# Optimization experiments

Hardware: AMD Instinct MI355X
Metric: run time of the kernel (lower is better)

The kernel has to match this reference:

```python
import jax, jax.numpy as jnp
import numpy as np
from jax import lax

B, H, W = 2, 240, 1216
ITER, NUM = 3, 9
CH = ITER * NUM  # 27


def setup_inputs() -> dict:
    key = jax.random.key(0)
    ks = jax.random.split(key, 6)
    inp = jax.random.normal(ks[0], (B, 1, H, W), dtype=jnp.float32)
    guide = jax.random.normal(ks[1], (B, CH, H, W), dtype=jnp.float32)
    sp_dep = jax.random.uniform(ks[2], (B, 1, H, W), dtype=jnp.float32)
    confidence = jax.random.normal(ks[3], (B, 1, H, W), dtype=jnp.float32)
    conv_w = jax.random.normal(ks[4], (3 * CH, CH, 3, 3), dtype=jnp.float32) * 0.05
    conv_b = jax.random.normal(ks[5], (3 * CH,), dtype=jnp.float32) * 0.05
    # fixed 3x3 tap offsets, rows are (dx, dy) -- matches mode='xy'
    tap = jnp.array([[-1, -1], [0, -1], [1, -1], [-1, 0], [0, 0], [1, 0], [-1, 1], [0, 1], [1, 1]], dtype=jnp.float32)
    return {"input": inp, "guide": guide, "sp_dep": sp_dep, "confidence": confidence,
            "conv_w": conv_w, "conv_b": conv_b, "tap": tap}


def _bilinear_zeros(img, px, py):
    """img: [B,H,W]; px,py: [B,N,H,W] pixel coords. Matches F.grid_sample
    (bilinear, padding_mode='zeros', align_corners=False): the normalized grid
    built in get_refgrid maps exactly to pixel coord = x + tap + offset."""
    Hh, Ww = img.shape[-2], img.shape[-1]
    x0f = jnp.floor(px)
    y0f = jnp.floor(py)
    wx1 = px - x0f
    wy1 = py - y0f
    x0 = x0f.astype(jnp.int32)
    y0 = y0f.astype(jnp.int32)
    flat = img.reshape(img.shape[0], Hh * Ww)

    def gather(xi, yi):
        valid = (xi >= 0) & (xi < Ww) & (yi >= 0) & (yi < Hh)
        idx = jnp.clip(yi, 0, Hh - 1) * Ww + jnp.clip(xi, 0, Ww - 1)
        v = jax.vmap(lambda f, i: f[i])(flat, idx)  # [B,N,H,W]
        return jnp.where(valid, v, jnp.zeros((), img.dtype))

    v00 = gather(x0, y0)
    v01 = gather(x0 + 1, y0)
    v10 = gather(x0, y0 + 1)
    v11 = gather(x0 + 1, y0 + 1)
    return ((1 - wy1) * ((1 - wx1) * v00 + wx1 * v01)
            + wy1 * ((1 - wx1) * v10 + wx1 * v11))


def reference(input, guide, sp_dep, confidence, conv_w, conv_b, tap):
    Bb, _, Hh, Ww = input.shape
    out = lax.conv_general_dilated(
        guide, conv_w, window_strides=(1, 1), padding=((1, 1), (1, 1)),
        dimension_numbers=("NCHW", "OIHW", "NCHW")) + conv_b[None, :, None, None]
    # split into offsets (2*ch) and affinities (ch)
    offset = out[:, :2 * CH].reshape(Bb, ITER, NUM, 2, Hh, Ww)  # b iter n (x,y) h w
    aff = out[:, 2 * CH:].reshape(Bb, ITER, NUM, Hh, Ww)
    aff = jax.nn.softmax(aff, axis=2)  # softmax over the NUM taps

    conf = jax.nn.sigmoid(confidence[:, 0]) * jnp.sign(sp_dep[:, 0])  # [B,H,W]
    spd = sp_dep[:, 0]

    xg = jnp.arange(Ww, dtype=jnp.float32)
    yg = jnp.arange(Hh, dtype=jnp.float32)
    # sampling pixel coords: x + tap_x + offset_x  (exact grid_sample equivalence)
    px = offset[:, :, :, 0] + tap[None, None, :, 0, None, None] + xg[None, None, None, None, :]
    py = offset[:, :, :, 1] + tap[None, None, :, 1, None, None] + yg[None, None, None, :, None]

    cur = input[:, 0]  # [B,H,W]
    feat_init = cur
    inter = []
    for i in range(ITER):
        vals = _bilinear_zeros(cur, px[:, i], py[:, i])  # [B,NUM,H,W]
        agg = jnp.sum(vals * aff[:, i], axis=1)          # affinity-weighted sum
        cur = (1 - conf) * agg + conf * spd
        inter.append(cur)
    pred = cur[:, None]
    return pred, feat_init[:, None], jnp.stack(inter, axis=0)[:, :, None]
```

## Files before the change

### kernel.cpp

```cpp
#include <hip/hip_runtime.h>
#include <math.h>

#define B_ 2
#define H_ 240
#define W_ 1216
#define CH_ 27
#define NUM_ 9
#define PIX_ (B_ * H_ * W_)
#define CHP 32
#define CHL 40
#define TX 32
#define TY 8
#define HALO_W (TX + 2)
#define HALO_H (TY + 2)
#define GH 8
#define HS_W (TX + 2 * GH + 1)
#define HS_H (TY + 2 * GH + 1)
#define GT_ELEMS (HALO_H * HALO_W * 4)
#define SC_ELEMS (HS_H * HS_W)

typedef __attribute__((ext_vector_type(8))) __bf16 bf16x8;
typedef __attribute__((ext_vector_type(16))) float f32x16;

__global__ __launch_bounds__(256) void transpose_guide(
    const float* __restrict__ guide, __bf16* __restrict__ gt)
{
    int pix = blockIdx.x * 256 + threadIdx.x;
    if (pix >= PIX_) return;
    int b = pix / (H_ * W_);
    int off = pix - b * (H_ * W_);
    __align__(16) __bf16 tmp[CHP];
    const float* src = guide + (size_t)b * CH_ * H_ * W_ + off;
    #pragma unroll
    for (int ic = 0; ic < CH_; ++ic)
        tmp[ic] = (__bf16)src[(size_t)ic * (H_ * W_)];
    #pragma unroll
    for (int ic = CH_; ic < CHP; ++ic) tmp[ic] = (__bf16)0.f;
    bf16x8* dst = (bf16x8*)(gt + (size_t)pix * CHP);
    const bf16x8* s8 = (const bf16x8*)tmp;
    #pragma unroll
    for (int c = 0; c < 4; ++c) dst[c] = s8[c];
}

__global__ __launch_bounds__(256) void prep_weights(
    const float* __restrict__ conv_w, __bf16* __restrict__ wlin)
{
    int idx = blockIdx.x * 256 + threadIdx.x;
    if (idx >= 3 * 9 * 2 * 64) return;
    int lane = idx & 63;
    int grp = idx >> 6;
    int ks = grp & 1;
    int tapi = (grp >> 1) % 9;
    int it = (grp >> 1) / 9;
    int n = lane & 31;
    int half = lane >> 5;
    __align__(16) __bf16 v8[8];
    #pragma unroll
    for (int j = 0; j < 8; ++j) {
        int ic = ks * 16 + half * 8 + j;
        float v = 0.f;
        if (ic < CH_ && n < CH_) {
            int oc = (n < 18) ? (it * 18 + n) : (54 + it * NUM_ + (n - 18));
            v = conv_w[(size_t)(oc * CH_ + ic) * 9 + tapi];
        }
        v8[j] = (__bf16)v;
    }
    *(bf16x8*)(wlin + (size_t)idx * 8) = *(const bf16x8*)v8;
}

__global__ __launch_bounds__(256, 3) void dyspn_iter_v7(
    const __bf16* __restrict__ gt, const __bf16* __restrict__ wlin,
    const float* __restrict__ conv_b, const float* __restrict__ tap,
    const float* __restrict__ confidence, const float* __restrict__ sp_dep,
    const float* __restrict__ cur_in, float* __restrict__ out_cur,
    float* __restrict__ pred, float* __restrict__ feat,
    const float* __restrict__ input, int iter)
{
    __shared__ __align__(16) __bf16 sG[HALO_H * HALO_W * CHL];
    __shared__ float sCur[HS_H * HS_W];

    const int tid = threadIdx.x;
    const int lane = tid & 63;
    const int w = tid >> 6;
    const int xl = lane & 31;
    const int half = lane >> 5;
    const int tileX0 = blockIdx.x * TX;
    const int tileY0 = blockIdx.y * TY;
    const int b = blockIdx.z;
    const size_t bbase = (size_t)b * (H_ * W_);
    const float* cur = cur_in + bbase;

    uint4 gv[6];
    #pragma unroll
    for (int k = 0; k < 6; ++k) {
        int idx = tid + k * 256;
        uint4 v = make_uint4(0, 0, 0, 0);
        if (idx < GT_ELEMS) {
            int chunk = idx & 3;
            int p = idx >> 2;
            int row = p / HALO_W;
            int px = p - row * HALO_W;
            int gy = tileY0 + row - 1;
            int gx = tileX0 + px - 1;
            if (gx >= 0 && gx < W_ && gy >= 0 && gy < H_) {
                size_t pg = bbase + (size_t)gy * W_ + gx;
                v = ((const uint4*)(gt + pg * CHP))[chunk];
            }
        }
        gv[k] = v;
    }

    const int winX0 = tileX0 - GH;
    const int winY0 = tileY0 - GH;
    float cv[5];
    #pragma unroll
    for (int k = 0; k < 5; ++k) {
        int idx = tid + k * 256;
        float v = 0.f;
        if (idx < SC_ELEMS) {
            int r = idx / HS_W;
            int cpos = idx - r * HS_W;
            int gy = winY0 + r;
            int gx = winX0 + cpos;
            if (gx >= 0 && gx < W_ && gy >= 0 && gy < H_)
                v = cur[(size_t)gy * W_ + gx];
        }
        cv[k] = v;
    }

    bf16x8 Bf[18];
    #pragma unroll
    for (int i = 0; i < 18; ++i)
        Bf[i] = *(const bf16x8*)(wlin + ((size_t)(iter * 18 + i) * 64 + lane) * 8);

    #pragma unroll
    for (int k = 0; k < 6; ++k) {
        int idx = tid + k * 256;
        if (idx < GT_ELEMS) {
            int chunk = idx & 3;
            int p = idx >> 2;
            *(uint4*)((char*)sG + ((size_t)(p * CHL) + chunk * 8) * 2) = gv[k];
        }
    }
    #pragma unroll
    for (int k = 0; k < 5; ++k) {
        int idx = tid + k * 256;
        if (idx < SC_ELEMS) sCur[idx] = cv[k];
    }
    __syncthreads();

    f32x16 acc0 = {0,0,0,0,0,0,0,0,0,0,0,0,0,0,0,0};
    f32x16 acc1 = {0,0,0,0,0,0,0,0,0,0,0,0,0,0,0,0};

    #pragma unroll
    for (int ks = 0; ks < 2; ++ks) {
        #pragma unroll
        for (int kw = 0; kw < 3; ++kw) {
            bf16x8 A4[4];
            #pragma unroll
            for (int d = 0; d < 4; ++d) {
                const __bf16* ap = sG + (size_t)((2 * w + d) * HALO_W + xl + kw) * CHL
                                 + ks * 16 + half * 8;
                A4[d] = *(const bf16x8*)ap;
            }
            #pragma unroll
            for (int kh = 0; kh < 3; ++kh) {
                int t = kh * 3 + kw;
                acc0 = __builtin_amdgcn_mfma_f32_32x32x16_bf16(Bf[t * 2 + ks], A4[kh],     acc0, 0, 0, 0);
                acc1 = __builtin_amdgcn_mfma_f32_32x32x16_bf16(Bf[t * 2 + ks], A4[kh + 1], acc1, 0, 0, 0);
            }
        }
    }

    float oth[16];
    #pragma unroll
    for (int r = 0; r < 16; ++r) {
        float send = half ? acc0[r] : acc1[r];
        oth[r] = __shfl_xor(send, 32, 64);
    }

    float v27[CH_];
    #pragma unroll
    for (int c = 0; c < CH_; ++c) {
        int r = (c & 3) + 4 * (c >> 3);
        int hc = (c >> 2) & 1;
        float own = half ? acc1[r] : acc0[r];
        float val = (hc == half) ? own : oth[r];
        int oc = (c < 18) ? (iter * 18 + c) : (54 + iter * NUM_ + (c - 18));
        v27[c] = val + conv_b[oc];
    }

    float m = v27[18];
    #pragma unroll
    for (int n = 1; n < 9; ++n) m = fmaxf(m, v27[18 + n]);
    float a[9]; float s = 0.f;
    #pragma unroll
    for (int n = 0; n < 9; ++n) { a[n] = __expf(v27[18 + n] - m); s += a[n]; }
    const float inv_s = 1.f / s;

    const int x = tileX0 + xl;
    const int y = tileY0 + 2 * w + half;
    float agg = 0.f;
    #pragma unroll
    for (int n = 0; n < 9; ++n) {
        float px = v27[2 * n]     + tap[2 * n]     + (float)x;
        float py = v27[2 * n + 1] + tap[2 * n + 1] + (float)y;
        float x0f = floorf(px), y0f = floorf(py);
        float wx = px - x0f, wy = py - y0f;
        int x0 = (int)x0f, y0 = (int)y0f;
        int lx = x0 - winX0, ly = y0 - winY0;
        float v00, v01, v10, v11;
        if ((unsigned)lx <= (unsigned)(HS_W - 2) && (unsigned)ly <= (unsigned)(HS_H - 2)) {
            int li = ly * HS_W + lx;
            v00 = sCur[li];
            v01 = sCur[li + 1];
            v10 = sCur[li + HS_W];
            v11 = sCur[li + HS_W + 1];
        } else {
            bool vx0 = (x0 >= 0) && (x0 < W_);
            bool vx1 = (x0 + 1 >= 0) && (x0 + 1 < W_);
            bool vy0 = (y0 >= 0) && (y0 < H_);
            bool vy1 = (y0 + 1 >= 0) && (y0 + 1 < H_);
            int cx0 = min(max(x0, 0), W_ - 1), cx1 = min(max(x0 + 1, 0), W_ - 1);
            int cy0 = min(max(y0, 0), H_ - 1), cy1 = min(max(y0 + 1, 0), H_ - 1);
            v00 = 0.f; v01 = 0.f; v10 = 0.f; v11 = 0.f;
            if (vy0) {
                const float* row = cur + (size_t)cy0 * W_;
                if (vx0) v00 = row[cx0];
                if (vx1) v01 = row[cx1];
            }
            if (vy1) {
                const float* row = cur + (size_t)cy1 * W_;
                if (vx0) v10 = row[cx0];
                if (vx1) v11 = row[cx1];
            }
        }
        float val = (1.f - wy) * ((1.f - wx) * v00 + wx * v01)
                  +        wy  * ((1.f - wx) * v10 + wx * v11);
        agg = fmaf(val, a[n] * inv_s, agg);
    }

    const int pix = b * (H_ * W_) + y * W_ + x;
    float c  = confidence[pix];
    float sp = sp_dep[pix];
    float sgn = (sp > 0.f) ? 1.f : ((sp < 0.f) ? -1.f : 0.f);
    float conf = sgn / (1.f + __expf(-c));
    float nc = (1.f - conf) * agg + conf * sp;

    out_cur[pix] = nc;
    if (pred) pred[pix] = nc;
    if (feat) feat[pix] = input[pix];
}

__global__ __launch_bounds__(256) void dyspn_iter_fp32(
    const float* __restrict__ guide, const float* __restrict__ conv_w,
    const float* __restrict__ conv_b, const float* __restrict__ tap,
    const float* __restrict__ confidence, const float* __restrict__ sp_dep,
    const float* __restrict__ cur_in, float* __restrict__ out_cur,
    float* __restrict__ pred, float* __restrict__ feat,
    const float* __restrict__ input, int iter)
{
    __shared__ float sg[CH_ * HALO_H * HALO_W];
    const int tid = threadIdx.x;
    const int tileX0 = blockIdx.x * TX;
    const int tileY0 = blockIdx.y * TY;
    const int b = blockIdx.z;
    for (int idx = tid; idx < CH_ * HALO_H * HALO_W; idx += 256) {
        int ic  = idx / (HALO_H * HALO_W);
        int rem = idx % (HALO_H * HALO_W);
        int ly = rem / HALO_W;
        int lx = rem % HALO_W;
        int gy = tileY0 + ly - 1;
        int gx = tileX0 + lx - 1;
        float v = 0.f;
        if (gx >= 0 && gx < W_ && gy >= 0 && gy < H_)
            v = guide[((b * CH_ + ic) * H_ + gy) * W_ + gx];
        sg[idx] = v;
    }
    __syncthreads();
    const int tx = tid % TX;
    const int ty = tid / TX;
    const int x = tileX0 + tx;
    const int y = tileY0 + ty;
    const int oc0 = iter * 18;
    const int oc1 = 54 + iter * NUM_;
    float acc[27];
    #pragma unroll
    for (int j = 0; j < 18; ++j) acc[j] = conv_b[oc0 + j];
    #pragma unroll
    for (int j = 0; j < 9; ++j)  acc[18 + j] = conv_b[oc1 + j];
    for (int ic = 0; ic < CH_; ++ic) {
        float g[9];
        #pragma unroll
        for (int t = 0; t < 9; ++t) {
            int dy = t / 3, dx = t % 3;
            g[t] = sg[ic * (HALO_H * HALO_W) + (ty + dy) * HALO_W + (tx + dx)];
        }
        #pragma unroll
        for (int j = 0; j < 18; ++j) {
            const float* wp = conv_w + ((oc0 + j) * CH_ + ic) * 9;
            #pragma unroll
            for (int t = 0; t < 9; ++t) acc[j] = fmaf(wp[t], g[t], acc[j]);
        }
        #pragma unroll
        for (int j = 0; j < 9; ++j) {
            const float* wp = conv_w + ((oc1 + j) * CH_ + ic) * 9;
            #pragma unroll
            for (int t = 0; t < 9; ++t) acc[18 + j] = fmaf(wp[t], g[t], acc[18 + j]);
        }
    }
    float m = acc[18];
    #pragma unroll
    for (int n = 1; n < 9; ++n) m = fmaxf(m, acc[18 + n]);
    float a[9]; float s = 0.f;
    #pragma unroll
    for (int n = 0; n < 9; ++n) { a[n] = __expf(acc[18 + n] - m); s += a[n]; }
    const float inv_s = 1.f / s;
    const float* cur = cur_in + b * (H_ * W_);
    float agg = 0.f;
    #pragma unroll
    for (int n = 0; n < 9; ++n) {
        float px = acc[2 * n]     + tap[2 * n]     + (float)x;
        float py = acc[2 * n + 1] + tap[2 * n + 1] + (float)y;
        float x0f = floorf(px), y0f = floorf(py);
        float wx = px - x0f, wy = py - y0f;
        int x0 = (int)x0f, y0 = (int)y0f;
        bool vx0 = (x0 >= 0) && (x0 < W_);
        bool vx1 = (x0 + 1 >= 0) && (x0 + 1 < W_);
        bool vy0 = (y0 >= 0) && (y0 < H_);
        bool vy1 = (y0 + 1 >= 0) && (y0 + 1 < H_);
        int cx0 = min(max(x0, 0), W_ - 1), cx1 = min(max(x0 + 1, 0), W_ - 1);
        int cy0 = min(max(y0, 0), H_ - 1), cy1 = min(max(y0 + 1, 0), H_ - 1);
        float v00 = 0.f, v01 = 0.f, v10 = 0.f, v11 = 0.f;
        if (vy0) {
            const float* row = cur + cy0 * W_;
            if (vx0) v00 = row[cx0];
            if (vx1) v01 = row[cx1];
        }
        if (vy1) {
            const float* row = cur + cy1 * W_;
            if (vx0) v10 = row[cx0];
            if (vx1) v11 = row[cx1];
        }
        float val = (1.f - wy) * ((1.f - wx) * v00 + wx * v01)
                  +        wy  * ((1.f - wx) * v10 + wx * v11);
        agg = fmaf(val, a[n] * inv_s, agg);
    }
    const int pix = b * (H_ * W_) + y * W_ + x;
    float c  = confidence[pix];
    float sp = sp_dep[pix];
    float sgn = (sp > 0.f) ? 1.f : ((sp < 0.f) ? -1.f : 0.f);
    float conf = sgn / (1.f + __expf(-c));
    float nc = (1.f - conf) * agg + conf * sp;
    out_cur[pix] = nc;
    if (pred) pred[pix] = nc;
    if (feat) feat[pix] = input[pix];
}

extern "C" void kernel_launch(void* const* d_in, const int* in_sizes, int n_in,
                              void* d_out, int out_size, void* d_ws, size_t ws_size,
                              hipStream_t stream) {
    (void)in_sizes; (void)n_in; (void)out_size;
    const float* input      = (const float*)d_in[0];
    const float* guide      = (const float*)d_in[1];
    const float* sp_dep     = (const float*)d_in[2];
    const float* confidence = (const float*)d_in[3];
    const float* conv_w     = (const float*)d_in[4];
    const float* conv_b     = (const float*)d_in[5];
    const float* tap        = (const float*)d_in[6];

    float* out   = (float*)d_out;
    const int P  = PIX_;
    float* pred  = out;
    float* feat  = out + P;
    float* inter = out + 2 * P;

    dim3 grid(W_ / TX, H_ / TY, B_);
    dim3 block(256);

    const size_t gt_bytes   = (size_t)PIX_ * CHP * 2;
    const size_t wlin_bytes = (size_t)3 * 9 * 2 * 64 * 8 * 2;

    if (ws_size >= gt_bytes + wlin_bytes) {
        __bf16* gt   = (__bf16*)d_ws;
        __bf16* wlin = (__bf16*)((char*)d_ws + gt_bytes);

        transpose_guide<<<(PIX_ + 255) / 256, 256, 0, stream>>>(guide, gt);
        prep_weights<<<(3 * 9 * 2 * 64 + 255) / 256, 256, 0, stream>>>(conv_w, wlin);

        for (int i = 0; i < 3; ++i) {
            const float* cur = (i == 0) ? input : (inter + (i - 1) * P);
            dyspn_iter_v7<<<grid, block, 0, stream>>>(
                gt, wlin, conv_b, tap, confidence, sp_dep,
                cur, inter + i * P,
                (i == 2) ? pred : nullptr,
                (i == 0) ? feat : nullptr,
                input, i);
        }
    } else {
        for (int i = 0; i < 3; ++i) {
            const float* cur = (i == 0) ? input : (inter + (i - 1) * P);
            dyspn_iter_fp32<<<grid, block, 0, stream>>>(
                guide, conv_w, conv_b, tap, confidence, sp_dep,
                cur, inter + i * P,
                (i == 2) ? pred : nullptr,
                (i == 0) ? feat : nullptr,
                input, i);
        }
    }
}
```

Measured before the change: 187.4 us.

## Fuse guide transpose into iteration kernel, loading fp32 guide directly per tile

Removes the separate transpose_guide pass that converted the guide to a padded channel-last bf16 buffer, and instead has each iteration kernel load the fp32 guide halo directly, convert it to bf16 and scatter it into the channel-last shared-memory tile. This drops one kernel launch and the intermediate workspace buffer. In exchange, each of the three iterations now reads fp32 channel-planar data (twice the bytes of bf16), holds 36 values per thread in registers, and performs scalar 2-byte shared-memory stores plus a padding-zero pass.

```diff
diff --git a/kernel.cpp b/kernel.cpp
--- a/kernel.cpp
+++ b/kernel.cpp
@@ -7,40 +7,19 @@
 #define CH_ 27
 #define NUM_ 9
 #define PIX_ (B_ * H_ * W_)
-#define CHP 32
 #define CHL 40
 #define TX 32
 #define TY 8
 #define HALO_W (TX + 2)
 #define HALO_H (TY + 2)
+#define G_ELEMS (CH_ * HALO_H * HALO_W)
 #define GH 8
 #define HS_W (TX + 2 * GH + 1)
 #define HS_H (TY + 2 * GH + 1)
-#define GT_ELEMS (HALO_H * HALO_W * 4)
 #define SC_ELEMS (HS_H * HS_W)
 
 typedef __attribute__((ext_vector_type(8))) __bf16 bf16x8;
 typedef __attribute__((ext_vector_type(16))) float f32x16;
-
-__global__ __launch_bounds__(256) void transpose_guide(
-    const float* __restrict__ guide, __bf16* __restrict__ gt)
-{
-    int pix = blockIdx.x * 256 + threadIdx.x;
-    if (pix >= PIX_) return;
-    int b = pix / (H_ * W_);
-    int off = pix - b * (H_ * W_);
-    __align__(16) __bf16 tmp[CHP];
-    const float* src = guide + (size_t)b * CH_ * H_ * W_ + off;
-    #pragma unroll
-    for (int ic = 0; ic < CH_; ++ic)
-        tmp[ic] = (__bf16)src[(size_t)ic * (H_ * W_)];
-    #pragma unroll
-    for (int ic = CH_; ic < CHP; ++ic) tmp[ic] = (__bf16)0.f;
-    bf16x8* dst = (bf16x8*)(gt + (size_t)pix * CHP);
-    const bf16x8* s8 = (const bf16x8*)tmp;
-    #pragma unroll
-    for (int c = 0; c < 4; ++c) dst[c] = s8[c];
-}
 
 __global__ __launch_bounds__(256) void prep_weights(
     const float* __restrict__ conv_w, __bf16* __restrict__ wlin)
@@ -68,8 +47,8 @@
     *(bf16x8*)(wlin + (size_t)idx * 8) = *(const bf16x8*)v8;
 }
 
-__global__ __launch_bounds__(256, 3) void dyspn_iter_v7(
-    const __bf16* __restrict__ gt, const __bf16* __restrict__ wlin,
+__global__ __launch_bounds__(256, 3) void dyspn_iter_v8(
+    const float* __restrict__ guide, const __bf16* __restrict__ wlin,
     const float* __restrict__ conv_b, const float* __restrict__ tap,
     const float* __restrict__ confidence, const float* __restrict__ sp_dep,
     const float* __restrict__ cur_in, float* __restrict__ out_cur,
@@ -89,25 +68,24 @@
     const int b = blockIdx.z;
     const size_t bbase = (size_t)b * (H_ * W_);
     const float* cur = cur_in + bbase;
-
-    uint4 gv[6];
-    #pragma unroll
-    for (int k = 0; k < 6; ++k) {
+    const float* gb  = guide + (size_t)b * CH_ * H_ * W_;
+
+    float gval[36];
+    #pragma unroll
+    for (int k = 0; k < 36; ++k) {
         int idx = tid + k * 256;
-        uint4 v = make_uint4(0, 0, 0, 0);
-        if (idx < GT_ELEMS) {
-            int chunk = idx & 3;
-            int p = idx >> 2;
-            int row = p / HALO_W;
-            int px = p - row * HALO_W;
-            int gy = tileY0 + row - 1;
-            int gx = tileX0 + px - 1;
-            if (gx >= 0 && gx < W_ && gy >= 0 && gy < H_) {
-                size_t pg = bbase + (size_t)gy * W_ + gx;
-                v = ((const uint4*)(gt + pg * CHP))[chunk];
-            }
-        }
-        gv[k] = v;
+        int i2 = (idx < G_ELEMS) ? idx : (G_ELEMS - 1);
+        int ic  = i2 / (HALO_H * HALO_W);
+        int rem = i2 - ic * (HALO_H * HALO_W);
+        int row = rem / HALO_W;
+        int px  = rem - row * HALO_W;
+        int gy = tileY0 + row - 1;
+        int gx = tileX0 + px - 1;
+        bool ok = (gx >= 0) && (gx < W_) && (gy >= 0) && (gy < H_);
+        int cy = min(max(gy, 0), H_ - 1);
+        int cx = min(max(gx, 0), W_ - 1);
+        float v = gb[((size_t)ic * H_ + cy) * W_ + cx];
+        gval[k] = ok ? v : 0.f;
     }
 
     const int winX0 = tileX0 - GH;
@@ -134,13 +112,18 @@
         Bf[i] = *(const bf16x8*)(wlin + ((size_t)(iter * 18 + i) * 64 + lane) * 8);
 
     #pragma unroll
-    for (int k = 0; k < 6; ++k) {
+    for (int k = 0; k < 36; ++k) {
         int idx = tid + k * 256;
-        if (idx < GT_ELEMS) {
-            int chunk = idx & 3;
-            int p = idx >> 2;
-            *(uint4*)((char*)sG + ((size_t)(p * CHL) + chunk * 8) * 2) = gv[k];
-        }
+        if (idx < G_ELEMS) {
+            int ic  = idx / (HALO_H * HALO_W);
+            int rem = idx - ic * (HALO_H * HALO_W);
+            sG[rem * CHL + ic] = (__bf16)gval[k];
+        }
+    }
+    for (int idx = tid; idx < HALO_H * HALO_W * 5; idx += 256) {
+        int rem = idx / 5;
+        int ic  = CH_ + (idx - rem * 5);
+        sG[rem * CHL + ic] = (__bf16)0.f;
     }
     #pragma unroll
     for (int k = 0; k < 5; ++k) {
@@ -378,20 +361,17 @@
     dim3 grid(W_ / TX, H_ / TY, B_);
     dim3 block(256);
 
-    const size_t gt_bytes   = (size_t)PIX_ * CHP * 2;
     const size_t wlin_bytes = (size_t)3 * 9 * 2 * 64 * 8 * 2;
 
-    if (ws_size >= gt_bytes + wlin_bytes) {
-        __bf16* gt   = (__bf16*)d_ws;
-        __bf16* wlin = (__bf16*)((char*)d_ws + gt_bytes);
-
-        transpose_guide<<<(PIX_ + 255) / 256, 256, 0, stream>>>(guide, gt);
+    if (ws_size >= wlin_bytes) {
+        __bf16* wlin = (__bf16*)d_ws;
+
         prep_weights<<<(3 * 9 * 2 * 64 + 255) / 256, 256, 0, stream>>>(conv_w, wlin);
 
         for (int i = 0; i < 3; ++i) {
             const float* cur = (i == 0) ? input : (inter + (i - 1) * P);
-            dyspn_iter_v7<<<grid, block, 0, stream>>>(
-                gt, wlin, conv_b, tap, confidence, sp_dep,
+            dyspn_iter_v8<<<grid, block, 0, stream>>>(
+                guide, wlin, conv_b, tap, confidence, sp_dep,
                 cur, inter + i * P,
                 (i == 2) ? pred : nullptr,
                 (i == 0) ? feat : nullptr,
```

Result: slower. 365.8 us (+95.2%).
